# Performance work log

Measured on AMD Instinct MI355X. Metric: run time of the kernel, lower is better.

Reference implementation:

```python
import jax, jax.numpy as jnp
import numpy as np

D = 384            # d_model
NUM_CLUSTERS = 100
MOM = 0.95         # cluster EMA momentum
ALPHA = 0.02 * (64.0 / D) ** 0.5  # SemanticMemoryLatentSpace alpha schedule
B = 512            # number of items processed sequentially
NORM_CAP = 50.0    # Frobenius-norm saturation threshold


def setup_inputs() -> dict:
    key = jax.random.key(0)
    k1, k2 = jax.random.split(key)
    embeddings = jax.random.normal(k1, (B, D), dtype=jnp.float32)
    # AdaptiveMemoryKernel init: L = randn*0.1 ; K0 = L L^T + 0.1 I (SPD-ish)
    L = jax.random.normal(k2, (D, D), dtype=jnp.float32) * 0.1
    kernel_init = L @ L.T + 0.1 * jnp.eye(D, dtype=jnp.float32)
    return {"embeddings": embeddings, "kernel_init": kernel_init}


def _forward(embeddings, kernel_init):
    def step(carry, e):
        K, prev_norm, count, C, cnts, active = carry
        # --- SemanticNoveltyTracker.compute_novelty: cosine sim vs active centroids ---
        e_norm = jnp.linalg.norm(e)
        c_norms = jnp.linalg.norm(C, axis=1)              # [num_clusters]
        sims = (C @ e) / (c_norms * e_norm + 1e-8)        # vectorized cosine sims
        mask = jnp.arange(NUM_CLUSTERS) < active
        sims_m = jnp.where(mask, sims, -2.0)              # mask inactive clusters
        max_sim = jnp.max(sims_m)
        closest = jnp.argmax(sims_m)
        novelty = jnp.where(active == 0, 1.0, 1.0 - max_sim ** 2)
        novelty = jnp.clip(novelty, 0.0, 1.0)
        # --- AdaptiveMemoryKernel.update_kernel ---
        pert = jnp.outer(e, e)                            # symmetric by construction
        tr = jnp.trace(pert)
        pert = jnp.where(tr > 1e-8, pert / jnp.maximum(tr, 1e-8) * D, pert)
        iw = novelty ** 1.5                               # squared-novelty weighting
        norm_before = jnp.linalg.norm(K)
        growth = jnp.where((count > 0) & (prev_norm > 0),
                           (norm_before - prev_norm) / jnp.maximum(prev_norm, 1e-12), 0.0)
        a = jnp.where(growth < 0.01, ALPHA * 1.5, ALPHA)  # boost when plateauing
        K = K + (a * iw) * pert
        K = (K + K.T) * 0.5                               # symmetrize
        kn = jnp.linalg.norm(K)
        K = jnp.where(kn > NORM_CAP, K / kn * NORM_CAP, K)  # soft saturation clip
        new_norm = jnp.linalg.norm(K)
        # --- SemanticNoveltyTracker.update_cluster ---
        create_new = (novelty > 0.7) & (active < NUM_CLUSTERS)
        idx = jnp.where(create_new, active, closest).astype(jnp.int32)
        old = C[idx]
        newc = jnp.where(create_new, e, MOM * old + (1.0 - MOM) * e)
        C = C.at[idx].set(newc)
        cnts = cnts.at[idx].set(jnp.where(create_new, 1.0, cnts[idx] + 1.0))
        active = active + create_new.astype(jnp.int32)
        return (K, new_norm, count + 1, C, cnts, active), None

    C0 = jnp.zeros((NUM_CLUSTERS, D), dtype=embeddings.dtype)
    cnts0 = jnp.zeros((NUM_CLUSTERS,), dtype=embeddings.dtype)
    init = (kernel_init, jnp.float32(0.0), jnp.int32(0), C0, cnts0, jnp.int32(0))
    (K, _, _, _, _, _), _ = jax.lax.scan(step, init, embeddings)
    # space warping: apply evolved kernel to the batch
    refined = embeddings @ K                              # [B, D]
    return refined


def reference(embeddings, kernel_init):
    return _forward(embeddings, kernel_init)
```

## Files before the change

### kernel.cpp

```cpp
#include <hip/hip_runtime.h>


#define A_BOOSTF 0.012247448713915891f

template <int CTRL>
__device__ __forceinline__ float dpp_f(float x) {
  return __int_as_float(
      __builtin_amdgcn_mov_dpp(__float_as_int(x), CTRL, 0xf, 0xf, true));
}
template <int CTRL>
__device__ __forceinline__ unsigned dpp_u(unsigned x) {
  return (unsigned)__builtin_amdgcn_mov_dpp((int)x, CTRL, 0xf, 0xf, true);
}
__device__ __forceinline__ float rdlane_f(float x, int l) {
  return __int_as_float(__builtin_amdgcn_readlane(__float_as_int(x), l));
}
__device__ __forceinline__ unsigned rdlane_u(unsigned x, int l) {
  return (unsigned)__builtin_amdgcn_readlane((int)x, l);
}
__device__ __forceinline__ float wave_sum64(float v) {
  v += dpp_f<0xB1>(v);
  v += dpp_f<0x4E>(v);
  v += dpp_f<0x124>(v);
  v += dpp_f<0x128>(v);
  return (rdlane_f(v, 0) + rdlane_f(v, 16)) + (rdlane_f(v, 32) + rdlane_f(v, 48));
}
__device__ __forceinline__ unsigned sortable(float v) {
  unsigned u = __float_as_uint(v);
  return u ^ (unsigned)(((int)u >> 31) | 0x80000000);
}
__device__ __forceinline__ float unsortable(unsigned x) {
  unsigned u = (x & 0x80000000u) ? (x ^ 0x80000000u) : ~x;
  return __uint_as_float(u);
}
__device__ __forceinline__ unsigned wave_umax64(unsigned v) {
  v = max(v, dpp_u<0xB1>(v));
  v = max(v, dpp_u<0x4E>(v));
  v = max(v, dpp_u<0x124>(v));
  v = max(v, dpp_u<0x128>(v));
  return max(max(rdlane_u(v, 0), rdlane_u(v, 16)),
             max(rdlane_u(v, 32), rdlane_u(v, 48)));
}

#define GXC(K, D)                                                              \
  ((D) < 4 ? ((D) == 0   ? gxq[K][0].x                                         \
              : (D) == 1 ? gxq[K][0].y                                         \
              : (D) == 2 ? gxq[K][0].z                                         \
                         : gxq[K][0].w)                                        \
   : (D) < 8                                                                   \
       ? ((D) == 4   ? gxq[K][1].x                                             \
          : (D) == 5 ? gxq[K][1].y                                             \
          : (D) == 6 ? gxq[K][1].z                                             \
                     : gxq[K][1].w)                                            \
   : (D) < 12 ? ((D) == 8    ? gxq[K][2].x                                     \
                 : (D) == 9  ? gxq[K][2].y                                     \
                 : (D) == 10 ? gxq[K][2].z                                     \
                             : gxq[K][2].w)                                    \
              : ((D) == 12   ? gxq[K][3].x                                     \
                 : (D) == 13 ? gxq[K][3].y                                     \
                 : (D) == 14 ? gxq[K][3].z                                     \
                             : gxq[K][3].w))

__global__ __launch_bounds__(256) void gemm_nt(const float* __restrict__ A,
                                               const float* __restrict__ B,
                                               float* __restrict__ C,
                                               int N, int K) {
  __shared__ float As[32][33];
  __shared__ float Bs[32][33];
  int bx = blockIdx.x, by = blockIdx.y;
  int tid = threadIdx.x;
  int tx = tid & 15, ty = tid >> 4;
  float a00 = 0.f, a01 = 0.f, a10 = 0.f, a11 = 0.f;
  for (int k0 = 0; k0 < K; k0 += 32) {
    for (int l = tid; l < 1024; l += 256) {
      int r = l >> 5, c = l & 31;
      As[r][c] = A[(by * 32 + r) * K + k0 + c];
      Bs[r][c] = B[(bx * 32 + r) * K + k0 + c];
    }
    __syncthreads();
#pragma unroll
    for (int k = 0; k < 32; ++k) {
      float x0 = As[2 * ty][k], x1 = As[2 * ty + 1][k];
      float y0 = Bs[2 * tx][k], y1 = Bs[2 * tx + 1][k];
      a00 += x0 * y0; a01 += x0 * y1; a10 += x1 * y0; a11 += x1 * y1;
    }
    __syncthreads();
  }
  int i = by * 32 + 2 * ty, jj = bx * 32 + 2 * tx;
  C[i * N + jj] = a00;           C[i * N + jj + 1] = a01;
  C[(i + 1) * N + jj] = a10;     C[(i + 1) * N + jj + 1] = a11;
}

__global__ __launch_bounds__(256) void gemm_nn(const float* __restrict__ A,
                                               const float* __restrict__ B,
                                               float* __restrict__ C,
                                               int N, int K) {
  __shared__ float As[32][33];
  __shared__ float Bs[32][33];
  int bx = blockIdx.x, by = blockIdx.y;
  int tid = threadIdx.x;
  int tx = tid & 15, ty = tid >> 4;
  float a00 = 0.f, a01 = 0.f, a10 = 0.f, a11 = 0.f;
  for (int k0 = 0; k0 < K; k0 += 32) {
    for (int l = tid; l < 1024; l += 256) {
      int r = l >> 5, c = l & 31;
      As[r][c] = A[(by * 32 + r) * K + k0 + c];
      Bs[r][c] = B[(k0 + r) * N + bx * 32 + c];
    }
    __syncthreads();
#pragma unroll
    for (int k = 0; k < 32; ++k) {
      float x0 = As[2 * ty][k], x1 = As[2 * ty + 1][k];
      float y0 = Bs[k][2 * tx], y1 = Bs[k][2 * tx + 1];
      a00 += x0 * y0; a01 += x0 * y1; a10 += x1 * y0; a11 += x1 * y1;
    }
    __syncthreads();
  }
  int i = by * 32 + 2 * ty, jj = bx * 32 + 2 * tx;
  C[i * N + jj] = a00;           C[i * N + jj + 1] = a01;
  C[(i + 1) * N + jj] = a10;     C[(i + 1) * N + jj + 1] = a11;
}

__global__ __launch_bounds__(256) void final_gemm(const float* __restrict__ G,
                                                  const float* __restrict__ E,
                                                  const float* __restrict__ M0,
                                                  const float* __restrict__ W,
                                                  const float* __restrict__ gS,
                                                  float* __restrict__ out) {
  __shared__ float As[32][33];
  __shared__ float Bs[32][33];
  int bx = blockIdx.x, by = blockIdx.y;
  int tid = threadIdx.x;
  int tx = tid & 15, ty = tid >> 4;
  float a00 = 0.f, a01 = 0.f, a10 = 0.f, a11 = 0.f;
  for (int k0 = 0; k0 < 512; k0 += 32) {
    for (int l = tid; l < 1024; l += 256) {
      int r = l >> 5, c = l & 31;
      As[r][c] = G[(by * 32 + r) * 512 + k0 + c] * W[k0 + c];
      Bs[r][c] = E[(k0 + r) * 384 + bx * 32 + c];
    }
    __syncthreads();
#pragma unroll
    for (int k = 0; k < 32; ++k) {
      float x0 = As[2 * ty][k], x1 = As[2 * ty + 1][k];
      float y0 = Bs[k][2 * tx], y1 = Bs[k][2 * tx + 1];
      a00 += x0 * y0; a01 += x0 * y1; a10 += x1 * y0; a11 += x1 * y1;
    }
    __syncthreads();
  }
  float gv = gS[0];
  int i = by * 32 + 2 * ty, jj = bx * 32 + 2 * tx;
  out[i * 384 + jj]         = gv * M0[i * 384 + jj]         + a00;
  out[i * 384 + jj + 1]     = gv * M0[i * 384 + jj + 1]     + a01;
  out[(i + 1) * 384 + jj]     = gv * M0[(i + 1) * 384 + jj]     + a10;
  out[(i + 1) * 384 + jj + 1] = gv * M0[(i + 1) * 384 + jj + 1] + a11;
}

__global__ __launch_bounds__(256) void prep_kernel(const float* __restrict__ E,
                                                   const float* __restrict__ M0,
                                                   const float* __restrict__ K0,
                                                   float* __restrict__ u,
                                                   float* __restrict__ Kpart) {
  __shared__ double wr[4];
  int b = blockIdx.x;
  int tid = threadIdx.x, lane = tid & 63, wv = tid >> 6;
  if (b < 128) {
    int row = b * 4 + wv;
    const float4* e4 = (const float4*)(E + row * 384);
    const float4* m4 = (const float4*)(M0 + row * 384);
    float p = 0.f;
    for (int i = lane; i < 96; i += 64) {
      float4 a = e4[i], bb = m4[i];
      p += a.x * bb.x + a.y * bb.y + a.z * bb.z + a.w * bb.w;
    }
#pragma unroll
    for (int off = 32; off; off >>= 1) p += __shfl_down(p, off);
    if (lane == 0) u[row] = p;
  } else {
    int cb = b - 128;
    const float* p = K0 + cb * 2304 + tid * 9;
    double acc = 0.0;
#pragma unroll
    for (int i = 0; i < 9; ++i) { double v = (double)p[i]; acc += v * v; }
#pragma unroll
    for (int off = 32; off; off >>= 1) acc += __shfl_down(acc, off);
    if (lane == 0) wr[wv] = acc;
    __syncthreads();
    if (tid == 0) Kpart[cb] = (float)(wr[0] + wr[1] + wr[2] + wr[3]);
  }
}

__global__ __launch_bounds__(128) void scan_kernel(const float* __restrict__ G,
                                                   const float* __restrict__ u,
                                                   const float* __restrict__ Kpart,
                                                   float* __restrict__ Wout,
                                                   float* __restrict__ gOut) {
  __shared__ float RAW[100 * 257];
  __shared__ float gx_tbl[512 * 16];
  __shared__ float ren_tbl[512];
  __shared__ float u_sh[512];
  __shared__ float wh_sh[512];
  __shared__ float4 RING[512];
  __shared__ int FLAG;
  __shared__ int FLAG2;

  const int tid = threadIdx.x;
  const int wid = tid >> 6;
  const int lane = tid & 63;

  float4 z4 = {0.f, 0.f, 0.f, 0.f};
  for (int i = tid; i < 6425; i += 128) ((float4*)RAW)[i] = z4;
  for (int tt = tid; tt < 512; tt += 128) {
    const float* gr = G + tt * 512 + tt;
    const int lim = 512 - tt;
#pragma unroll
    for (int d = 0; d < 16; ++d)
      gx_tbl[tt * 16 + d] = (d < lim) ? gr[d] : 0.f;
    ren_tbl[tt] = __builtin_amdgcn_rcpf(__builtin_amdgcn_sqrtf(gr[0]));
  }
  if (tid < 128) ((float4*)u_sh)[tid] = ((const float4*)u)[tid];
  if (tid == 0) { FLAG = 0; FLAG2 = -1; }
  __syncthreads();

  if (wid == 0) {
    float d0 = 1.f, d1 = 1.f, cn0 = 0.f, cn1 = 0.f, s0 = 0.f, s1 = 0.f;
    int nact = 0;
    float r0[8], r1[8];
#pragma unroll
    for (int j = 0; j < 8; ++j) { r0[j] = 0.f; r1[j] = 0.f; }

#define W0STEP(K)                                                              \
    {                                                                          \
      float v0 = (lane < nact) ? s0 * renk[K] * r0[K] : -2.f;                  \
      float v1 = (lane + 64 < nact) ? s1 * renk[K] * r1[K] : -2.f;             \
      unsigned pk0 = (sortable(v0) & ~127u) | (unsigned)(127 - lane);          \
      unsigned pk1 = (sortable(v1) & ~127u) | (unsigned)(63 - lane);           \
      unsigned P = wave_umax64(max(pk0, pk1));                                 \
      int imax = 127 - (int)(P & 127u);                                        \
      float M = unsortable(P & ~127u);                                         \
      float nov = (nact == 0) ? 1.f : fminf(1.f, fmaxf(0.f, 1.f - M * M));     \
      int create = (nov > 0.7f && nact < 100) ? 1 : 0;                         \
      const int idxs = create ? nact : imax;                                   \
      const int cl = idxs & 63, hi = idxs >> 6;                                \
      float dcA = create ? 1.f : 0.95f * d0;                                   \
      float dcB = create ? 1.f : 0.95f * d1;                                   \
      float ccA = create ? trk[K]                                              \
                         : (0.9025f * cn0 + 0.095f * (d0 * r0[K]) +            \
                            0.0025f * trk[K]);                                 \
      float ccB = create ? trk[K]                                              \
                         : (0.9025f * cn1 + 0.095f * (d1 * r1[K]) +            \
                            0.0025f * trk[K]);                                 \
      float scA = dcA * __builtin_amdgcn_rcpf(__builtin_amdgcn_sqrtf(ccA));    \
      float scB = dcB * __builtin_amdgcn_rcpf(__builtin_amdgcn_sqrtf(ccB));    \
      float ivA = 0.05f * __builtin_amdgcn_rcpf(dcA);                          \
      float ivB = 0.05f * __builtin_amdgcn_rcpf(dcB);                          \
      bool own0 = (lane == cl) && (hi == 0);                                   \
      bool own1 = (lane == cl) && (hi == 1);                                   \
      d0 = own0 ? dcA : d0; cn0 = own0 ? ccA : cn0; s0 = own0 ? scA : s0;      \
      d1 = own1 ? dcB : d1; cn1 = own1 ? ccB : cn1; s1 = own1 ? scB : s1;      \
      float bnew = create ? 1.f : rdlane_f(hi ? ivB : ivA, cl);                \
      nact += create;                                                          \
      float pb0 = own0 ? bnew : 0.f, pb1 = own1 ? bnew : 0.f;                  \
      _Pragma("unroll") for (int j = (K) + 1; j < 8; ++j) {                    \
        r0[j] += pb0 * GXC(K, (j) - (K));                                      \
        r1[j] += pb1 * GXC(K, (j) - (K));                                      \
      }                                                                        \
      bnewA[K] = bnew; novA[K] = nov; idxA[K] = idxs;                          \
      pb0A[K] = pb0; pb1A[K] = pb1;                                            \
    }

    for (int R = 0; R < 64; ++R) {
      const int t = 8 * R;
      const int c = t & 255;
      const int tn = t + 8;
      const int cnx = tn & 255;

      if (t == 256) {
        while (__hip_atomic_load(&FLAG2, __ATOMIC_ACQUIRE,
                                 __HIP_MEMORY_SCOPE_WORKGROUP) < 31)
          __builtin_amdgcn_s_sleep(1);
        for (int i = lane; i < 6425; i += 64) ((float4*)RAW)[i] = z4;
        __builtin_amdgcn_sched_barrier(0);
        const float* Gb = G + 256;
        float A[4][4], Bv[4][4];
        float4 SA[4], SB[4];
#pragma unroll
        for (int j = 0; j < 4; ++j) {
#pragma unroll
          for (int m = 0; m < 4; ++m) A[j][m] = Gb[j * 512 + m * 64 + lane];
          SA[j] = RING[j];
        }
        for (int s = 0; s < 256; s += 8) {
#pragma unroll
          for (int j = 0; j < 4; ++j) {
#pragma unroll
            for (int m = 0; m < 4; ++m)
              Bv[j][m] = Gb[(s + 4 + j) * 512 + m * 64 + lane];
            SB[j] = RING[s + 4 + j];
          }
#pragma unroll
          for (int j = 0; j < 4; ++j) {
            float bh = SA[j].x; int id = __float_as_int(SA[j].y);
#pragma unroll
            for (int m = 0; m < 4; ++m) {
              const int a_ = id * 257 + m * 64 + lane;
              RAW[a_] += bh * A[j][m];
            }
          }
          if (s + 8 < 256) {
#pragma unroll
            for (int j = 0; j < 4; ++j) {
#pragma unroll
              for (int m = 0; m < 4; ++m)
                A[j][m] = Gb[(s + 8 + j) * 512 + m * 64 + lane];
              SA[j] = RING[s + 8 + j];
            }
          }
#pragma unroll
          for (int j = 0; j < 4; ++j) {
            float bh = SB[j].x; int id = __float_as_int(SB[j].y);
#pragma unroll
            for (int m = 0; m < 4; ++m) {
              const int a_ = id * 257 + m * 64 + lane;
              RAW[a_] += bh * Bv[j][m];
            }
          }
        }
        __builtin_amdgcn_sched_barrier(0);
#pragma unroll
        for (int j = 0; j < 8; ++j) r0[j] = RAW[lane * 257 + j];
        if (lane < 36) {
#pragma unroll
          for (int j = 0; j < 8; ++j) r1[j] = RAW[(lane + 64) * 257 + j];
        }
        __builtin_amdgcn_sched_barrier(0);
      }

      float4 gxq[8][4];
      float trk[8], renk[8];
#pragma unroll
      for (int k = 0; k < 8; ++k) {
        const float4* gp = (const float4*)(gx_tbl + (t + k) * 16);
        gxq[k][0] = gp[0]; gxq[k][1] = gp[1];
        gxq[k][2] = gp[2]; gxq[k][3] = gp[3];
        trk[k] = gxq[k][0].x;
        renk[k] = ren_tbl[t + k];
      }

      float bnewA[8], novA[8], pb0A[8], pb1A[8];
      int idxA[8];

      W0STEP(0) W0STEP(1) W0STEP(2) W0STEP(3)

      float r0n[8], r1n[8];
      const bool doRead = (tn < 512) && (cnx != 0);
      if (doRead) {
        while (__hip_atomic_load(&FLAG2, __ATOMIC_ACQUIRE,
                                 __HIP_MEMORY_SCOPE_WORKGROUP) < R - 1)
          __builtin_amdgcn_s_sleep(1);
#pragma unroll
        for (int j = 0; j < 8; ++j) r0n[j] = RAW[lane * 257 + cnx + j];
        if (lane < 36) {
#pragma unroll
          for (int j = 0; j < 8; ++j) r1n[j] = RAW[(lane + 64) * 257 + cnx + j];
        } else {
#pragma unroll
          for (int j = 0; j < 8; ++j) r1n[j] = 0.f;
        }
      }

      W0STEP(4) W0STEP(5) W0STEP(6) W0STEP(7)

      if (doRead) {
#pragma unroll
        for (int j = 0; j < 8; ++j) {
          float pa = 0.f, pb = 0.f;
#pragma unroll
          for (int k = 0; k < 8; ++k) {
            pa += pb0A[k] * GXC(k, 8 + (j) - (k));
            pb += pb1A[k] * GXC(k, 8 + (j) - (k));
          }
          r0[j] = r0n[j] + pa;
          r1[j] = r1n[j] + pb;
        }
      }

      if (lane == 0) {
#pragma unroll
        for (int k = 0; k < 8; ++k) {
          float4 r4; r4.x = bnewA[k]; r4.y = __int_as_float(idxA[k]);
          r4.z = novA[k]; r4.w = 0.f;
          RING[t + k] = r4;
        }
        __hip_atomic_store(&FLAG, R + 1, __ATOMIC_RELEASE,
                           __HIP_MEMORY_SCOPE_WORKGROUP);
      }
    }
#undef W0STEP
  } else {
    float q8[8];
#pragma unroll
    for (int gI = 0; gI < 8; ++gI) q8[gI] = 0.f;
    float n2 = wave_sum64(Kpart[lane]);
    float g = 1.f, ginv = 1.f;

    for (int r = 0; r < 64; ++r) {
      const int t = 8 * r;
      const int c = t & 255;
      const int gbase = (t >> 6) & ~3;

      float B[8][8];
#pragma unroll
      for (int k = 0; k < 8; ++k)
#pragma unroll
        for (int gI = 0; gI < 8; ++gI)
          B[k][gI] = G[(t + k) * 512 + gI * 64 + lane];

      while (__hip_atomic_load(&FLAG, __ATOMIC_ACQUIRE,
                               __HIP_MEMORY_SCOPE_WORKGROUP) < r + 1)
        __builtin_amdgcn_s_sleep(1);

      float4 rgv[8];
#pragma unroll
      for (int k = 0; k < 8; ++k) rgv[k] = RING[t + k];

#pragma unroll
      for (int k = 0; k < 8; ++k) {
        float bnew = rgv[k].x;
        int id = __float_as_int(rgv[k].y);
#pragma unroll
        for (int mg = 0; mg < 4; ++mg)
          if (mg * 64 + 63 >= c) {
            const int a_ = id * 257 + mg * 64 + lane;
            RAW[a_] += bnew * B[k][gbase + mg];
          }
      }
      __hip_atomic_store(&FLAG2, r, __ATOMIC_RELEASE,
                         __HIP_MEMORY_SCOPE_WORKGROUP);

      float trm[8], gxw[8][8];
#pragma unroll
      for (int m = 0; m < 8; ++m) {
        trm[m] = gx_tbl[(t + m) * 16];
#pragma unroll
        for (int j = m + 1; j < 8; ++j)
          gxw[m][j] = gx_tbl[(t + m) * 16 + (j - m)];
      }
      float4 uuA = *(const float4*)&u_sh[t];
      float4 uuB = *(const float4*)&u_sh[t + 4];
      float um[8] = {uuA.x, uuA.y, uuA.z, uuA.w, uuB.x, uuB.y, uuB.z, uuB.w};

      const int grp = t >> 6;
      float qsel = q8[0];
#pragma unroll
      for (int gI = 1; gI < 8; ++gI) qsel = (grp == gI) ? q8[gI] : qsel;
      float qeff[8];
#pragma unroll
      for (int k = 0; k < 8; ++k) qeff[k] = rdlane_f(qsel, (t & 63) + k);

      float wh[8];
#pragma unroll
      for (int m = 0; m < 8; ++m) {
        float nov = rgv[m].z;
        float iw = nov * __builtin_amdgcn_sqrtf(nov);
        float psc = 384.0f * __builtin_amdgcn_rcpf(fmaxf(trm[m], 1e-8f));
        float ccf = A_BOOSTF * iw * psc;
        float qv = g * (um[m] + qeff[m]);
        float n2n = n2 + 2.f * ccf * qv + ccf * ccf * trm[m] * trm[m];
        float kn = __builtin_amdgcn_sqrtf(n2n);
        float fct = (kn > 50.f) ? 50.f * __builtin_amdgcn_rcpf(kn) : 1.f;
        float fiv = (kn > 50.f) ? kn * 0.02f : 1.f;
        wh[m] = ccf * ginv;
        n2 = n2n * fct * fct; g *= fct; ginv *= fiv;
#pragma unroll
        for (int j = m + 1; j < 8; ++j)
          qeff[j] += wh[m] * gxw[m][j] * gxw[m][j];
      }

      if (lane == 0) {
#pragma unroll
        for (int m = 0; m < 8; ++m) wh_sh[t + m] = wh[m];
      }
#pragma unroll
      for (int gI = 0; gI < 8; ++gI)
#pragma unroll
        for (int k = 0; k < 8; ++k)
          q8[gI] += wh[k] * B[k][gI] * B[k][gI];
    }

    for (int s2 = lane; s2 < 512; s2 += 64) Wout[s2] = wh_sh[s2] * g;
    if (lane == 0) gOut[0] = g;
  }
}

extern "C" void kernel_launch(void* const* d_in, const int* in_sizes, int n_in,
                              void* d_out, int out_size, void* d_ws,
                              size_t ws_size, hipStream_t stream) {
  const float* E = (const float*)d_in[0];
  const float* K0 = (const float*)d_in[1];
  float* out = (float*)d_out;

  float* G = (float*)d_ws;
  float* M0 = G + 512 * 512;
  float* u = M0 + 512 * 384;
  float* W = u + 512;
  float* gS = W + 512;
  float* Kpart = gS + 1;

  gemm_nt<<<dim3(16, 16), 256, 0, stream>>>(E, E, G, 512, 384);
  gemm_nn<<<dim3(12, 16), 256, 0, stream>>>(E, K0, M0, 384, 384);
  prep_kernel<<<192, 256, 0, stream>>>(E, M0, K0, u, Kpart);
  scan_kernel<<<1, 128, 0, stream>>>(G, u, Kpart, W, gS);
  final_gemm<<<dim3(12, 16), 256, 0, stream>>>(G, E, M0, W, gS, out);
}
```

Baseline: 302.5 us.

## Split scan consumer into separate RAW-update and norm-tracking waves

Raises the scan block from two to three waves. A dedicated wave now does the RAW accumulation while another does the kernel-norm and weight recurrence, so the two no longer run serially in one consumer wave. The serial leader wave prefetches next-step gram rows one step ahead, accumulates the cross-block partials incrementally, and the float4 ring is split into separate arrays. This shortens the critical path of the sequential scan, at the cost of an extra wave polling the flags and more register pressure in the leader.

Result: faster. 259.8 us (-14.1%).

```diff
diff --git a/kernel.cpp b/kernel.cpp
--- a/kernel.cpp
+++ b/kernel.cpp
@@ -42,24 +42,24 @@
              max(rdlane_u(v, 32), rdlane_u(v, 48)));
 }
 
-#define GXC(K, D)                                                              \
-  ((D) < 4 ? ((D) == 0   ? gxq[K][0].x                                         \
-              : (D) == 1 ? gxq[K][0].y                                         \
-              : (D) == 2 ? gxq[K][0].z                                         \
-                         : gxq[K][0].w)                                        \
+#define GX(D)                                                                  \
+  ((D) < 4 ? ((D) == 0   ? gq[0].x                                             \
+              : (D) == 1 ? gq[0].y                                             \
+              : (D) == 2 ? gq[0].z                                             \
+                         : gq[0].w)                                            \
    : (D) < 8                                                                   \
-       ? ((D) == 4   ? gxq[K][1].x                                             \
-          : (D) == 5 ? gxq[K][1].y                                             \
-          : (D) == 6 ? gxq[K][1].z                                             \
-                     : gxq[K][1].w)                                            \
-   : (D) < 12 ? ((D) == 8    ? gxq[K][2].x                                     \
-                 : (D) == 9  ? gxq[K][2].y                                     \
-                 : (D) == 10 ? gxq[K][2].z                                     \
-                             : gxq[K][2].w)                                    \
-              : ((D) == 12   ? gxq[K][3].x                                     \
-                 : (D) == 13 ? gxq[K][3].y                                     \
-                 : (D) == 14 ? gxq[K][3].z                                     \
-                             : gxq[K][3].w))
+       ? ((D) == 4   ? gq[1].x                                                 \
+          : (D) == 5 ? gq[1].y                                                 \
+          : (D) == 6 ? gq[1].z                                                 \
+                     : gq[1].w)                                                \
+   : (D) < 12 ? ((D) == 8    ? gq[2].x                                         \
+                 : (D) == 9  ? gq[2].y                                         \
+                 : (D) == 10 ? gq[2].z                                         \
+                             : gq[2].w)                                        \
+              : ((D) == 12   ? gq[3].x                                         \
+                 : (D) == 13 ? gq[3].y                                         \
+                 : (D) == 14 ? gq[3].z                                         \
+                             : gq[3].w))
 
 __global__ __launch_bounds__(256) void gemm_nt(const float* __restrict__ A,
                                                const float* __restrict__ B,
@@ -190,7 +190,7 @@
   }
 }
 
-__global__ __launch_bounds__(128) void scan_kernel(const float* __restrict__ G,
+__global__ __launch_bounds__(192) void scan_kernel(const float* __restrict__ G,
                                                    const float* __restrict__ u,
                                                    const float* __restrict__ Kpart,
                                                    float* __restrict__ Wout,
@@ -200,7 +200,9 @@
   __shared__ float ren_tbl[512];
   __shared__ float u_sh[512];
   __shared__ float wh_sh[512];
-  __shared__ float4 RING[512];
+  __shared__ float RG_bnew[512];
+  __shared__ float RG_nov[512];
+  __shared__ int RG_idx[512];
   __shared__ int FLAG;
   __shared__ int FLAG2;
 
@@ -209,8 +211,8 @@
   const int lane = tid & 63;
 
   float4 z4 = {0.f, 0.f, 0.f, 0.f};
-  for (int i = tid; i < 6425; i += 128) ((float4*)RAW)[i] = z4;
-  for (int tt = tid; tt < 512; tt += 128) {
+  for (int i = tid; i < 6425; i += 192) ((float4*)RAW)[i] = z4;
+  for (int tt = tid; tt < 512; tt += 192) {
     const float* gr = G + tt * 512 + tt;
     const int lim = 512 - tt;
 #pragma unroll
@@ -229,10 +231,22 @@
 #pragma unroll
     for (int j = 0; j < 8; ++j) { r0[j] = 0.f; r1[j] = 0.f; }
 
+    const float4* gx4 = (const float4*)gx_tbl;
+    float4 gq[4];
+    float renk;
+    gq[0] = gx4[0]; gq[1] = gx4[1]; gq[2] = gx4[2]; gq[3] = gx4[3];
+    renk = ren_tbl[0];
+
 #define W0STEP(K)                                                              \
     {                                                                          \
-      float v0 = (lane < nact) ? s0 * renk[K] * r0[K] : -2.f;                  \
-      float v1 = (lane + 64 < nact) ? s1 * renk[K] * r1[K] : -2.f;             \
+                                \
+      const int tnx = (t + (K) + 1 < 512) ? t + (K) + 1 : 511;                 \
+      float4 gqn0 = gx4[tnx * 4], gqn1 = gx4[tnx * 4 + 1];                     \
+      float4 gqn2 = gx4[tnx * 4 + 2], gqn3 = gx4[tnx * 4 + 3];                 \
+      float renn = ren_tbl[tnx];                                               \
+      const float trk = gq[0].x;                                               \
+      float v0 = (lane < nact) ? s0 * renk * r0[K] : -2.f;                     \
+      float v1 = (lane + 64 < nact) ? s1 * renk * r1[K] : -2.f;                \
       unsigned pk0 = (sortable(v0) & ~127u) | (unsigned)(127 - lane);          \
       unsigned pk1 = (sortable(v1) & ~127u) | (unsigned)(63 - lane);           \
       unsigned P = wave_umax64(max(pk0, pk1));                                 \
@@ -244,12 +258,12 @@
       const int cl = idxs & 63, hi = idxs >> 6;                                \
       float dcA = create ? 1.f : 0.95f * d0;                                   \
       float dcB = create ? 1.f : 0.95f * d1;                                   \
-      float ccA = create ? trk[K]                                              \
+      float ccA = create ? trk                                                 \
                          : (0.9025f * cn0 + 0.095f * (d0 * r0[K]) +            \
-                            0.0025f * trk[K]);                                 \
-      float ccB = create ? trk[K]                                              \
+                            0.0025f * trk);                                    \
+      float ccB = create ? trk                                                 \
                          : (0.9025f * cn1 + 0.095f * (d1 * r1[K]) +            \
-                            0.0025f * trk[K]);                                 \
+                            0.0025f * trk);                                    \
       float scA = dcA * __builtin_amdgcn_rcpf(__builtin_amdgcn_sqrtf(ccA));    \
       float scB = dcB * __builtin_amdgcn_rcpf(__builtin_amdgcn_sqrtf(ccB));    \
       float ivA = 0.05f * __builtin_amdgcn_rcpf(dcA);                          \
@@ -262,16 +276,20 @@
       nact += create;                                                          \
       float pb0 = own0 ? bnew : 0.f, pb1 = own1 ? bnew : 0.f;                  \
       _Pragma("unroll") for (int j = (K) + 1; j < 8; ++j) {                    \
-        r0[j] += pb0 * GXC(K, (j) - (K));                                      \
-        r1[j] += pb1 * GXC(K, (j) - (K));                                      \
+        r0[j] += pb0 * GX((j) - (K));                                          \
+        r1[j] += pb1 * GX((j) - (K));                                          \
+      }                                                                        \
+      _Pragma("unroll") for (int j = 0; j < 8; ++j) {                          \
+        pa0[j] += pb0 * GX(8 + (j) - (K));                                     \
+        pa1[j] += pb1 * GX(8 + (j) - (K));                                     \
       }                                                                        \
       bnewA[K] = bnew; novA[K] = nov; idxA[K] = idxs;                          \
-      pb0A[K] = pb0; pb1A[K] = pb1;                                            \
+      gq[0] = gqn0; gq[1] = gqn1; gq[2] = gqn2; gq[3] = gqn3;                  \
+      renk = renn;                                                             \
     }
 
     for (int R = 0; R < 64; ++R) {
       const int t = 8 * R;
-      const int c = t & 255;
       const int tn = t + 8;
       const int cnx = tn & 255;
 
@@ -283,12 +301,13 @@
         __builtin_amdgcn_sched_barrier(0);
         const float* Gb = G + 256;
         float A[4][4], Bv[4][4];
-        float4 SA[4], SB[4];
+        float ab[4], bb[4];
+        int ai[4], bi[4];
 #pragma unroll
         for (int j = 0; j < 4; ++j) {
 #pragma unroll
           for (int m = 0; m < 4; ++m) A[j][m] = Gb[j * 512 + m * 64 + lane];
-          SA[j] = RING[j];
+          ab[j] = RG_bnew[j]; ai[j] = RG_idx[j];
         }
         for (int s = 0; s < 256; s += 8) {
 #pragma unroll
@@ -296,15 +315,14 @@
 #pragma unroll
             for (int m = 0; m < 4; ++m)
               Bv[j][m] = Gb[(s + 4 + j) * 512 + m * 64 + lane];
-            SB[j] = RING[s + 4 + j];
+            bb[j] = RG_bnew[s + 4 + j]; bi[j] = RG_idx[s + 4 + j];
           }
 #pragma unroll
           for (int j = 0; j < 4; ++j) {
-            float bh = SA[j].x; int id = __float_as_int(SA[j].y);
 #pragma unroll
             for (int m = 0; m < 4; ++m) {
-              const int a_ = id * 257 + m * 64 + lane;
-              RAW[a_] += bh * A[j][m];
+              const int a_ = ai[j] * 257 + m * 64 + lane;
+              RAW[a_] += ab[j] * A[j][m];
             }
           }
           if (s + 8 < 256) {
@@ -313,16 +331,15 @@
 #pragma unroll
               for (int m = 0; m < 4; ++m)
                 A[j][m] = Gb[(s + 8 + j) * 512 + m * 64 + lane];
-              SA[j] = RING[s + 8 + j];
+              ab[j] = RG_bnew[s + 8 + j]; ai[j] = RG_idx[s + 8 + j];
             }
           }
 #pragma unroll
           for (int j = 0; j < 4; ++j) {
-            float bh = SB[j].x; int id = __float_as_int(SB[j].y);
 #pragma unroll
             for (int m = 0; m < 4; ++m) {
-              const int a_ = id * 257 + m * 64 + lane;
-              RAW[a_] += bh * Bv[j][m];
+              const int a_ = bi[j] * 257 + m * 64 + lane;
+              RAW[a_] += bb[j] * Bv[j][m];
             }
           }
         }
@@ -336,28 +353,20 @@
         __builtin_amdgcn_sched_barrier(0);
       }
 
-      float4 gxq[8][4];
-      float trk[8], renk[8];
-#pragma unroll
-      for (int k = 0; k < 8; ++k) {
-        const float4* gp = (const float4*)(gx_tbl + (t + k) * 16);
-        gxq[k][0] = gp[0]; gxq[k][1] = gp[1];
-        gxq[k][2] = gp[2]; gxq[k][3] = gp[3];
-        trk[k] = gxq[k][0].x;
-        renk[k] = ren_tbl[t + k];
-      }
-
-      float bnewA[8], novA[8], pb0A[8], pb1A[8];
+      float bnewA[8], novA[8];
       int idxA[8];
+      float pa0[8], pa1[8];
+#pragma unroll
+      for (int j = 0; j < 8; ++j) { pa0[j] = 0.f; pa1[j] = 0.f; }
 
       W0STEP(0) W0STEP(1) W0STEP(2) W0STEP(3)
-
-      float r0n[8], r1n[8];
-      const bool doRead = (tn < 512) && (cnx != 0);
-      if (doRead) {
+      W0STEP(4) W0STEP(5) W0STEP(6) W0STEP(7)
+
+      if (tn < 512 && cnx != 0) {
         while (__hip_atomic_load(&FLAG2, __ATOMIC_ACQUIRE,
                                  __HIP_MEMORY_SCOPE_WORKGROUP) < R - 1)
           __builtin_amdgcn_s_sleep(1);
+        float r0n[8], r1n[8];
 #pragma unroll
         for (int j = 0; j < 8; ++j) r0n[j] = RAW[lane * 257 + cnx + j];
         if (lane < 36) {
@@ -367,76 +376,83 @@
 #pragma unroll
           for (int j = 0; j < 8; ++j) r1n[j] = 0.f;
         }
-      }
-
-      W0STEP(4) W0STEP(5) W0STEP(6) W0STEP(7)
-
-      if (doRead) {
 #pragma unroll
         for (int j = 0; j < 8; ++j) {
-          float pa = 0.f, pb = 0.f;
-#pragma unroll
-          for (int k = 0; k < 8; ++k) {
-            pa += pb0A[k] * GXC(k, 8 + (j) - (k));
-            pb += pb1A[k] * GXC(k, 8 + (j) - (k));
-          }
-          r0[j] = r0n[j] + pa;
-          r1[j] = r1n[j] + pb;
+          r0[j] = r0n[j] + pa0[j];
+          r1[j] = r1n[j] + pa1[j];
         }
       }
+      __builtin_amdgcn_sched_barrier(0);
 
       if (lane == 0) {
 #pragma unroll
         for (int k = 0; k < 8; ++k) {
-          float4 r4; r4.x = bnewA[k]; r4.y = __int_as_float(idxA[k]);
-          r4.z = novA[k]; r4.w = 0.f;
-          RING[t + k] = r4;
+          RG_bnew[t + k] = bnewA[k];
+          RG_nov[t + k] = novA[k];
+          RG_idx[t + k] = idxA[k];
         }
         __hip_atomic_store(&FLAG, R + 1, __ATOMIC_RELEASE,
                            __HIP_MEMORY_SCOPE_WORKGROUP);
       }
     }
 #undef W0STEP
-  } else {
-    float q8[8];
-#pragma unroll
-    for (int gI = 0; gI < 8; ++gI) q8[gI] = 0.f;
-    float n2 = wave_sum64(Kpart[lane]);
-    float g = 1.f, ginv = 1.f;
-
+  } else if (wid == 1) {
     for (int r = 0; r < 64; ++r) {
       const int t = 8 * r;
       const int c = t & 255;
       const int gbase = (t >> 6) & ~3;
 
-      float B[8][8];
+      float B4[8][4];
 #pragma unroll
       for (int k = 0; k < 8; ++k)
 #pragma unroll
-        for (int gI = 0; gI < 8; ++gI)
-          B[k][gI] = G[(t + k) * 512 + gI * 64 + lane];
+        for (int mg = 0; mg < 4; ++mg)
+          B4[k][mg] = G[(t + k) * 512 + (gbase + mg) * 64 + lane];
 
       while (__hip_atomic_load(&FLAG, __ATOMIC_ACQUIRE,
                                __HIP_MEMORY_SCOPE_WORKGROUP) < r + 1)
         __builtin_amdgcn_s_sleep(1);
 
-      float4 rgv[8];
-#pragma unroll
-      for (int k = 0; k < 8; ++k) rgv[k] = RING[t + k];
+      float bn[8];
+      int id[8];
+#pragma unroll
+      for (int k = 0; k < 8; ++k) { bn[k] = RG_bnew[t + k]; id[k] = RG_idx[t + k]; }
 
 #pragma unroll
       for (int k = 0; k < 8; ++k) {
-        float bnew = rgv[k].x;
-        int id = __float_as_int(rgv[k].y);
 #pragma unroll
         for (int mg = 0; mg < 4; ++mg)
           if (mg * 64 + 63 >= c) {
-            const int a_ = id * 257 + mg * 64 + lane;
-            RAW[a_] += bnew * B[k][gbase + mg];
+            const int a_ = id[k] * 257 + mg * 64 + lane;
+            RAW[a_] += bn[k] * B4[k][mg];
           }
       }
       __hip_atomic_store(&FLAG2, r, __ATOMIC_RELEASE,
                          __HIP_MEMORY_SCOPE_WORKGROUP);
+    }
+  } else {
+    float q8[8];
+#pragma unroll
+    for (int gI = 0; gI < 8; ++gI) q8[gI] = 0.f;
+    float n2 = wave_sum64(Kpart[lane]);
+    float g = 1.f, ginv = 1.f;
+
+    for (int r = 0; r < 64; ++r) {
+      const int t = 8 * r;
+      float B[8][8];
+#pragma unroll
+      for (int k = 0; k < 8; ++k)
+#pragma unroll
+        for (int gI = 0; gI < 8; ++gI)
+          B[k][gI] = G[(t + k) * 512 + gI * 64 + lane];
+
+      while (__hip_atomic_load(&FLAG, __ATOMIC_ACQUIRE,
+                               __HIP_MEMORY_SCOPE_WORKGROUP) < r + 1)
+        __builtin_amdgcn_s_sleep(1);
+
+      float novv[8];
+#pragma unroll
+      for (int k = 0; k < 8; ++k) novv[k] = RG_nov[t + k];
 
       float trm[8], gxw[8][8];
 #pragma unroll
@@ -461,7 +477,7 @@
       float wh[8];
 #pragma unroll
       for (int m = 0; m < 8; ++m) {
-        float nov = rgv[m].z;
+        float nov = novv[m];
         float iw = nov * __builtin_amdgcn_sqrtf(nov);
         float psc = 384.0f * __builtin_amdgcn_rcpf(fmaxf(trm[m], 1e-8f));
         float ccf = A_BOOSTF * iw * psc;
@@ -510,6 +526,6 @@
   gemm_nt<<<dim3(16, 16), 256, 0, stream>>>(E, E, G, 512, 384);
   gemm_nn<<<dim3(12, 16), 256, 0, stream>>>(E, K0, M0, 384, 384);
   prep_kernel<<<192, 256, 0, stream>>>(E, M0, K0, u, Kpart);
-  scan_kernel<<<1, 128, 0, stream>>>(G, u, Kpart, W, gS);
+  scan_kernel<<<1, 192, 0, stream>>>(G, u, Kpart, W, gS);
   final_gemm<<<dim3(12, 16), 256, 0, stream>>>(G, E, M0, W, gS, out);
 }
```
